# Performance work log

Measured on AMD Instinct MI355X. Metric: run time of the kernel, lower is better.

Reference implementation:

```python
import jax, jax.numpy as jnp
import numpy as np

B, S, D = 2, 512, 256      # batch, seq_len, d_model
N = 16                     # d_state
DC = 4                     # d_conv
DI = 2 * D                 # d_inner
CHUNK = 32                 # scan remat chunk size (S % CHUNK == 0)


def setup_inputs() -> dict:
    key = jax.random.key(0)
    ks = jax.random.split(key, 10)
    sc = 0.02
    return {
        "x": jax.random.normal(ks[0], (B, S, D), jnp.float32),
        "adjacency_matrix": jax.random.uniform(ks[1], (B, S, S), dtype=jnp.float32),
        "ln_w": jnp.ones((D,), jnp.float32),
        "ln_b": jnp.zeros((D,), jnp.float32),
        "W_in": jax.random.normal(ks[2], (2 * DI, D), jnp.float32) * sc,
        "conv_w": jax.random.normal(ks[3], (DI, DI, DC), jnp.float32) * sc,
        "conv_b": jnp.zeros((DI,), jnp.float32),
        "W_xp": jax.random.normal(ks[4], (2 * N + 1, DI), jnp.float32) * sc,
        "W_dt": jax.random.normal(ks[5], (DI, 1), jnp.float32) * sc,
        "b_dt": jnp.zeros((DI,), jnp.float32),
        "Wr": jax.random.normal(ks[6], (N, N), jnp.float32) * sc,
        "br": jnp.zeros((N,), jnp.float32),
        "W_out": jax.random.normal(ks[7], (D, DI), jnp.float32) * sc,
    }


def _forward(x, adj, ln_w, ln_b, W_in, conv_w, conv_b, W_xp, W_dt, b_dt, Wr, br, W_out):
    residual = x
    # LayerNorm (biased variance, eps=1e-5, matching nn.LayerNorm)
    mu = x.mean(-1, keepdims=True)
    var = ((x - mu) ** 2).mean(-1, keepdims=True)
    xn = (x - mu) * jax.lax.rsqrt(var + 1e-5) * ln_w + ln_b
    # in_proj (no bias), chunk into x branch and gate z
    xz = xn @ W_in.T                                  # [B,S,2*DI]
    xp, z = xz[..., :DI], xz[..., DI:]
    # causal-ish conv1d with padding d_conv-1, then slice to seq_len
    xc = jax.lax.conv_general_dilated(
        xp.transpose(0, 2, 1), conv_w, (1,), [(DC - 1, DC - 1)],
        dimension_numbers=("NCH", "OIH", "NCH"))
    xc = (xc + conv_b[None, :, None])[..., :S].transpose(0, 2, 1)  # [B,S,DI]
    x_act = jax.nn.silu(xc)
    # x_proj (no bias) -> delta(1), B(N), C(N)
    ssm = x_act @ W_xp.T                              # [B,S,2N+1]
    delta = jax.nn.softplus(ssm[..., :1] @ W_dt.T + b_dt)  # [B,S,DI]
    Bm, Cm = ssm[..., 1:1 + N], ssm[..., 1 + N:]      # [B,S,N]
    pos = jnp.arange(S)

    def step(carry, xs):
        h, hist = xs_carry = carry
        t, d_t, B_t, C_t, x_t, a_t = xs
        # exponential-decay state update: h [B,DI,N]
        h = h * jnp.exp(-d_t)[..., None] + x_t[..., None] * B_t[:, None, :]
        # adjacency-gated, degree-normalized aggregation over prior states
        w = a_t * (pos < t)                           # [B,S], zeros for s>=t
        deg = jnp.maximum(w.sum(-1), 1.0)             # clamp(min=1.0)
        g = jnp.einsum('bs,sbdn->bdn', w, hist) / deg[:, None, None]
        boost = 0.1 * jax.nn.silu(g @ Wr.T + br)
        # torch skips the boost when t==0 or all causal weights are zero
        h = h + jnp.where((t > 0) & jnp.any(w > 0), boost, jnp.zeros_like(boost))
        hist = hist.at[t].set(h)
        y = jnp.einsum('bdn,bn->bd', h, C_t)
        return (h, hist), y

    xs = (pos,
          delta.transpose(1, 0, 2), Bm.transpose(1, 0, 2), Cm.transpose(1, 0, 2),
          x_act.transpose(1, 0, 2), adj.transpose(1, 0, 2))
    nchunks = S // CHUNK
    xs = jax.tree_util.tree_map(lambda a: a.reshape(nchunks, CHUNK, *a.shape[1:]), xs)
    carry0 = (jnp.zeros((B, DI, N), jnp.float32),
              jnp.zeros((S, B, DI, N), jnp.float32))

    @jax.checkpoint
    def chunk_body(carry, xs_c):
        return jax.lax.scan(step, carry, xs_c)

    _, ys = jax.lax.scan(chunk_body, carry0, xs)
    y = ys.reshape(S, B, DI).transpose(1, 0, 2)       # [B,S,DI]
    return (y * jax.nn.silu(z)) @ W_out.T + residual


def reference(x, adjacency_matrix, ln_w, ln_b, W_in, conv_w, conv_b, W_xp, W_dt, b_dt, Wr, br, W_out):
    return _forward(x, adjacency_matrix, ln_w, ln_b, W_in, conv_w, conv_b,
                    W_xp, W_dt, b_dt, Wr, br, W_out)
```

## Files before the change

kernel.cpp:

```cpp
#include <hip/hip_runtime.h>
#include <math.h>

static constexpr int B  = 2;
static constexpr int S  = 512;
static constexpr int D  = 256;
static constexpr int N  = 16;
static constexpr int DI = 512;
static constexpr int CHUNK = 32;
static constexpr int NCHUNK = S / CHUNK;
static constexpr int NL = NCHUNK / 2;
static constexpr int DN = DI * N;

typedef unsigned int uint32;
typedef unsigned short ushort16;
using bf16x8 = __attribute__((ext_vector_type(8))) short;
using f32x4  = __attribute__((ext_vector_type(4))) float;

__device__ __forceinline__ ushort16 f2bf(float f) {
    uint32 u = __float_as_uint(f);
    u = (u + 0x7fffu + ((u >> 16) & 1u)) >> 16;
    return (ushort16)u;
}
__device__ __forceinline__ float bflo(uint32 u) { return __uint_as_float(u << 16); }
__device__ __forceinline__ float bfhi(uint32 u) { return __uint_as_float(u & 0xffff0000u); }
__device__ __forceinline__ float bf2f(ushort16 u) { return __uint_as_float(((uint32)u) << 16); }
__device__ __forceinline__ uint32 pk2(float a, float b) {
    return (uint32)(ushort16)f2bf(a) | ((uint32)(ushort16)f2bf(b) << 16);
}
template<int K>
__device__ __forceinline__ float rork(float x) {
    return __uint_as_float((uint32)__builtin_amdgcn_mov_dpp(
        (int)__float_as_uint(x), 0x120 + K, 0xf, 0xf, false));
}

__global__ void ln_k(const float* __restrict__ x, const float* __restrict__ w,
                     const float* __restrict__ bias, ushort16* __restrict__ xnb) {
    int row = blockIdx.x;
    int lane = threadIdx.x;
    float4 v = *(const float4*)(x + row * D + lane * 4);
    float s = v.x + v.y + v.z + v.w;
    float q = v.x * v.x + v.y * v.y + v.z * v.z + v.w * v.w;
    for (int m = 1; m < 64; m <<= 1) { s += __shfl_xor(s, m); q += __shfl_xor(q, m); }
    float mu  = s * (1.0f / D);
    float var = q * (1.0f / D) - mu * mu;
    float rs  = rsqrtf(var + 1e-5f);
    float4 wv = *(const float4*)(w + lane * 4);
    float4 bv = *(const float4*)(bias + lane * 4);
    float4 o;
    o.x = (v.x - mu) * rs * wv.x + bv.x;
    o.y = (v.y - mu) * rs * wv.y + bv.y;
    o.z = (v.z - mu) * rs * wv.z + bv.z;
    o.w = (v.w - mu) * rs * wv.w + bv.w;
    uint2 pk;
    pk.x = pk2(o.x, o.y);
    pk.y = pk2(o.z, o.w);
    *(uint2*)(xnb + row * D + lane * 4) = pk;
}

template<int MODE>
__global__ __launch_bounds__(256) void gemmb_k(const ushort16* __restrict__ A,
                                               const float* __restrict__ W,
                                               const float* __restrict__ res,
                                               float* __restrict__ C,
                                               ushort16* __restrict__ xpb,
                                               float* __restrict__ zs,
                                               int M, int Nc, int K) {
    __shared__ __align__(16) short As[64 * 40];
    __shared__ __align__(16) short Ws[64 * 40];
    int tid = threadIdx.x;
    int l = tid & 63, wid = tid >> 6;
    int wm = wid & 1, wn = wid >> 1;
    int row0 = blockIdx.y * 64, col0 = blockIdx.x * 64;
    int r = tid >> 2, kseg = (tid & 3) * 8;
    f32x4 acc[2][2] = {};
    for (int k0 = 0; k0 < K; k0 += 32) {
        *(uint4*)&As[r * 40 + kseg] = *(const uint4*)(A + (size_t)(row0 + r) * K + k0 + kseg);
        {
            const float* wrow = W + (size_t)(col0 + r) * K + k0 + kseg;
            float4 w0 = *(const float4*)wrow;
            float4 w1 = *(const float4*)(wrow + 4);
            uint4 q;
            q.x = pk2(w0.x, w0.y); q.y = pk2(w0.z, w0.w);
            q.z = pk2(w1.x, w1.y); q.w = pk2(w1.z, w1.w);
            *(uint4*)&Ws[r * 40 + kseg] = q;
        }
        __syncthreads();
        bf16x8 aF[2], bF[2];
        #pragma unroll
        for (int am = 0; am < 2; ++am)
            aF[am] = *(const bf16x8*)&As[(wm * 32 + am * 16 + (l & 15)) * 40 + (l >> 4) * 8];
        #pragma unroll
        for (int bn = 0; bn < 2; ++bn)
            bF[bn] = *(const bf16x8*)&Ws[(wn * 32 + bn * 16 + (l & 15)) * 40 + (l >> 4) * 8];
        #pragma unroll
        for (int am = 0; am < 2; ++am)
            #pragma unroll
            for (int bn = 0; bn < 2; ++bn)
                acc[am][bn] = __builtin_amdgcn_mfma_f32_16x16x32_bf16(aF[am], bF[bn], acc[am][bn], 0, 0, 0);
        __syncthreads();
    }
    #pragma unroll
    for (int am = 0; am < 2; ++am)
        #pragma unroll
        for (int bn = 0; bn < 2; ++bn) {
            int cc = col0 + wn * 32 + bn * 16 + (l & 15);
            #pragma unroll
            for (int reg = 0; reg < 4; ++reg) {
                int rr = row0 + wm * 32 + am * 16 + (l >> 4) * 4 + reg;
                float v = acc[am][bn][reg];
                if (MODE == 0) {
                    if (res) v += res[(size_t)rr * Nc + cc];
                    C[(size_t)rr * Nc + cc] = v;
                } else {
                    int b = rr >> 9, t = rr & (S - 1);
                    if (cc < DI)
                        xpb[((size_t)(b * (S + 3) + 3 + t)) * DI + cc] = f2bf(v);
                    else
                        zs[((size_t)(b * S + t)) * DI + (cc - DI)] = v / (1.0f + __expf(-v));
                }
            }
        }
}

__global__ __launch_bounds__(256) void convm_k(const ushort16* __restrict__ xpb,
                                               const float* __restrict__ conv_w,
                                               const float* __restrict__ conv_b,
                                               float* __restrict__ x_act) {
    __shared__ __align__(16) short AxS[35 * 40];
    __shared__ __align__(16) short WbS[4 * 32 * 40];
    int tid = threadIdx.x;
    int l = tid & 63, wid = tid >> 6;
    int wm = wid & 1, wn = wid >> 1;
    int o0 = blockIdx.x * 32;
    int mt = blockIdx.y;
    int b = mt >> 4, tl0 = (mt & 15) * 32;
    f32x4 acc = {0.f, 0.f, 0.f, 0.f};

    for (int k0 = 0; k0 < DI; k0 += 32) {
        if (tid < 140) {
            int rr = tid >> 2, seg = tid & 3;
            uint4 v = *(const uint4*)(xpb + ((size_t)(b * (S + 3) + tl0 + rr)) * DI + k0 + seg * 8);
            *(uint4*)&AxS[rr * 40 + seg * 8] = v;
        }
        #pragma unroll
        for (int it = 0; it < 4; ++it) {
            int p = it * 256 + tid;
            int o = p >> 5, i = p & 31;
            float4 w4 = *(const float4*)(conv_w + ((size_t)(o0 + o) * DI + (k0 + i)) * 4);
            WbS[(0 * 32 + o) * 40 + i] = (short)f2bf(w4.x);
            WbS[(1 * 32 + o) * 40 + i] = (short)f2bf(w4.y);
            WbS[(2 * 32 + o) * 40 + i] = (short)f2bf(w4.z);
            WbS[(3 * 32 + o) * 40 + i] = (short)f2bf(w4.w);
        }
        __syncthreads();
        #pragma unroll
        for (int k = 0; k < 4; ++k) {
            bf16x8 aF = *(const bf16x8*)&AxS[(wm * 16 + (l & 15) + k) * 40 + (l >> 4) * 8];
            bf16x8 bF = *(const bf16x8*)&WbS[(k * 32 + wn * 16 + (l & 15)) * 40 + (l >> 4) * 8];
            acc = __builtin_amdgcn_mfma_f32_16x16x32_bf16(aF, bF, acc, 0, 0, 0);
        }
        __syncthreads();
    }
    int oc = o0 + wn * 16 + (l & 15);
    float bia = conv_b[oc];
    #pragma unroll
    for (int reg = 0; reg < 4; ++reg) {
        int m = wm * 16 + (l >> 4) * 4 + reg;
        float v = acc[reg] + bia;
        x_act[((size_t)(b * S + tl0 + m)) * DI + oc] = v / (1.0f + __expf(-v));
    }
}

__global__ void ssmE_k(const float* __restrict__ x_act, const float* __restrict__ W_xp,
                       const float* __restrict__ W_dt, const float* __restrict__ b_dt,
                       float* __restrict__ Bm, float* __restrict__ Cm,
                       float* __restrict__ E) {
    int row = blockIdx.x * 4 + (threadIdx.x >> 6);
    int lane = threadIdx.x & 63;
    const float* xr = x_act + (size_t)row * DI + lane * 8;
    float4 v0 = *(const float4*)xr;
    float4 v1 = *(const float4*)(xr + 4);
    float dtr = 0.0f;
    for (int j = 0; j < 2 * N + 1; ++j) {
        const float* wr = W_xp + (size_t)j * DI + lane * 8;
        float4 w0 = *(const float4*)wr;
        float4 w1 = *(const float4*)(wr + 4);
        float acc = v0.x * w0.x + v0.y * w0.y + v0.z * w0.z + v0.w * w0.w
                  + v1.x * w1.x + v1.y * w1.y + v1.z * w1.z + v1.w * w1.w;
        for (int m = 1; m < 64; m <<= 1) acc += __shfl_xor(acc, m);
        if (j == 0) dtr = acc;
        if (lane == 0) {
            if (j >= 1 && j < 1 + N) Bm[(size_t)row * N + (j - 1)] = acc;
            else if (j >= 1 + N)     Cm[(size_t)row * N + (j - 1 - N)] = acc;
        }
    }
    int d0 = lane * 8;
    float4 w0 = *(const float4*)(W_dt + d0);
    float4 w1 = *(const float4*)(W_dt + d0 + 4);
    float4 q0 = *(const float4*)(b_dt + d0);
    float4 q1 = *(const float4*)(b_dt + d0 + 4);
    float4 e0, e1;
    e0.x = 1.0f / (1.0f + __expf(dtr * w0.x + q0.x));
    e0.y = 1.0f / (1.0f + __expf(dtr * w0.y + q0.y));
    e0.z = 1.0f / (1.0f + __expf(dtr * w0.z + q0.z));
    e0.w = 1.0f / (1.0f + __expf(dtr * w0.w + q0.w));
    e1.x = 1.0f / (1.0f + __expf(dtr * w1.x + q1.x));
    e1.y = 1.0f / (1.0f + __expf(dtr * w1.y + q1.y));
    e1.z = 1.0f / (1.0f + __expf(dtr * w1.z + q1.z));
    e1.w = 1.0f / (1.0f + __expf(dtr * w1.w + q1.w));
    *(float4*)(E + (size_t)row * DI + d0) = e0;
    *(float4*)(E + (size_t)row * DI + d0 + 4) = e1;
}

__global__ void deg_k(const float* __restrict__ adj, float* __restrict__ rdeg, int* __restrict__ flagI) {
    int t = blockIdx.x & (S - 1), b = blockIdx.x >> 9;
    int lane = threadIdx.x;
    const float* row = adj + ((size_t)(b * S + t)) * S;
    float s = 0.0f; bool anyp = false;
    for (int i = lane; i < t; i += 64) { float v = row[i]; s += v; anyp |= (v > 0.0f); }
    for (int m = 1; m < 64; m <<= 1) s += __shfl_xor(s, m);
    bool any = __any(anyp);
    if (lane == 0) {
        rdeg[b * S + t] = 1.0f / fmaxf(s, 1.0f);
        if (t > 0 && any) atomicOr(flagI + t, 1);
    }
}

#define SCAN32(RO, ADJT, GSUM)                                              \
    _Pragma("unroll")                                                       \
    for (int j = 0; j < CHUNK; ++j) {                                       \
        float e  = eL [((RO) + j) * 8 + grp];                               \
        float xa = xaL[((RO) + j) * 8 + grp];                               \
        float Bn = BnL[((RO) + j) * 16 + n];                                \
        h = h * e + xa * Bn;                                                \
        float g0 = GSUM[j], g1 = 0.f, g2 = 0.f, g3 = 0.f;                   \
        const float* ar = (ADJT) + j * 36;                                  \
        int sp = 0;                                                         \
        _Pragma("unroll")                                                   \
        for (; sp + 4 <= j; sp += 4) {                                      \
            float4 av = *(const float4*)(ar + sp);                          \
            g0 += av.x * hreg[sp];     g1 += av.y * hreg[sp + 1];           \
            g2 += av.z * hreg[sp + 2]; g3 += av.w * hreg[sp + 3];           \
        }                                                                   \
        _Pragma("unroll")                                                   \
        for (; sp < j; ++sp) g0 += ar[sp] * hreg[sp];                       \
        float gr = (g0 + g1) + (g2 + g3);                                   \
        float m0 = gr * wrr[0] + rork<4>(gr) * wrr[4]                       \
                 + rork<8>(gr) * wrr[8] + rork<12>(gr) * wrr[12];           \
        float m1 = rork<1>(gr) * wrr[1] + rork<5>(gr) * wrr[5]              \
                 + rork<9>(gr) * wrr[9] + rork<13>(gr) * wrr[13];           \
        float m2 = rork<2>(gr) * wrr[2] + rork<6>(gr) * wrr[6]              \
                 + rork<10>(gr) * wrr[10] + rork<14>(gr) * wrr[14];         \
        float m3 = rork<3>(gr) * wrr[3] + rork<7>(gr) * wrr[7]              \
                 + rork<11>(gr) * wrr[11] + rork<15>(gr) * wrr[15];         \
        float acc = fmaf(rdegL[(RO) + j], (m0 + m1) + (m2 + m3), brn);      \
        if (flL[(RO) + j]) h += 0.1f * acc / (1.0f + __expf(-acc));         \
        hreg[j] = h;                                                        \
    }

#define PRESUM(GSUM, PTR) {                                                 \
    const ushort16* _p = (PTR);                                             \
    _Pragma("unroll")                                                       \
    for (int qi = 0; qi < 4; ++qi) {                                        \
        uint4 q = *(const uint4*)(_p + qi * 8);                             \
        GSUM[qi*8+0] += bflo(q.x); GSUM[qi*8+1] += bfhi(q.x);               \
        GSUM[qi*8+2] += bflo(q.y); GSUM[qi*8+3] += bfhi(q.y);               \
        GSUM[qi*8+4] += bflo(q.z); GSUM[qi*8+5] += bfhi(q.z);               \
        GSUM[qi*8+6] += bflo(q.w); GSUM[qi*8+7] += bfhi(q.w);               \
    } }

__global__ __launch_bounds__(256) void chunk2_k(const float* __restrict__ adj,
                                                const float* __restrict__ x_act,
                                                const float* __restrict__ E,
                                                const float* __restrict__ Bm,
                                                const float* __restrict__ rdeg,
                                                const int* __restrict__ flagI,
                                                const float* __restrict__ Wr,
                                                const float* __restrict__ br,
                                                ushort16* __restrict__ Gall,
                                                ushort16* __restrict__ histT,
                                                float* __restrict__ hlast, int lc) {
    __shared__ __align__(16) char smem[56320];
    int tid = threadIdx.x;
    int cbA = 2 * lc * CHUNK;
    int cbB = cbA + CHUNK;
    const size_t SLOT = (size_t)B * DN * 32;
    int rp = lc & 1, wp = (lc + 1) & 1;

    if (blockIdx.x < 128) {
        float* adjA  = (float*)smem;
        float* adjB  = (float*)(smem + 4608);
        short* AsM   = (short*)(smem + 9216);
        short* AsT   = (short*)(smem + 11776);
        float* eL    = (float*)(smem + 22016);
        float* xaL   = (float*)(smem + 24064);
        float* BnL   = (float*)(smem + 26112);
        float* rdegL = (float*)(smem + 30208);
        int*   flL   = (int*)  (smem + 30464);
        short* hTA   = (short*)(smem + 31232);
        float* Gmid  = (float*)(smem + 39424);
        short* hTB   = (short*)(smem + 39424);

        int b = blockIdx.x >> 6;
        int d0 = (blockIdx.x & 63) << 3;
        int n = tid & 15, grp = tid >> 4;
        int d = d0 + (grp & 7);
        int dn = d * N + n;
        int dnbase = (blockIdx.x & 63) << 7;

        {
            int j = tid >> 3, s4 = (tid & 7) * 4;
            {
                float4 a0 = *(const float4*)(adj + ((size_t)(b * S + cbA + j)) * S + cbA + s4);
                float* dp = adjA + j * 36 + s4;
                dp[0] = a0.x; dp[1] = a0.y; dp[2] = a0.z; dp[3] = a0.w;
            }
            {
                float4 a0 = *(const float4*)(adj + ((size_t)(b * S + cbB + j)) * S + cbB + s4);
                float* dp = adjB + j * 36 + s4;
                dp[0] = a0.x; dp[1] = a0.y; dp[2] = a0.z; dp[3] = a0.w;
            }
            {
                float4 a0 = *(const float4*)(adj + ((size_t)(b * S + cbB + j)) * S + cbA + s4);
                uint2 q; q.x = pk2(a0.x, a0.y); q.y = pk2(a0.z, a0.w);
                *(uint2*)&AsM[j * 40 + s4] = q;
            }
            if (lc < NL - 1) {
                #pragma unroll
                for (int st = 0; st < 4; ++st) {
                    int src = st >> 1, tgt = st & 1;
                    float4 a0 = *(const float4*)(adj + ((size_t)(b * S + cbA + 64 + 32 * tgt + j)) * S
                                                 + cbA + 32 * src + s4);
                    uint2 q; q.x = pk2(a0.x, a0.y); q.y = pk2(a0.z, a0.w);
                    *(uint2*)&AsT[(src * 2 + tgt) * 1280 + j * 40 + s4] = q;
                }
            }
            int jr = tid >> 2, dd = (tid & 3) * 2;
            float2 ev = *(const float2*)(E     + ((size_t)(b * S + cbA + jr)) * DI + d0 + dd);
            float2 xv = *(const float2*)(x_act + ((size_t)(b * S + cbA + jr)) * DI + d0 + dd);
            eL [jr * 8 + dd] = ev.x; eL [jr * 8 + dd + 1] = ev.y;
            xaL[jr * 8 + dd] = xv.x; xaL[jr * 8 + dd + 1] = xv.y;
            int nn = (tid & 3) * 4;
            float4 bv = *(const float4*)(Bm + ((size_t)(b * S + cbA + jr)) * N + nn);
            BnL[jr * 16 + nn] = bv.x; BnL[jr * 16 + nn + 1] = bv.y;
            BnL[jr * 16 + nn + 2] = bv.z; BnL[jr * 16 + nn + 3] = bv.w;
            if (tid < 64) {
                rdegL[tid] = rdeg[b * S + cbA + tid];
                flL[tid]   = flagI[cbA + tid];
            }
        }
        __syncthreads();
        if (tid >= 128) return;

        float gsA[CHUNK], gsB[CHUNK];
        #pragma unroll
        for (int j = 0; j < CHUNK; ++j) { gsA[j] = 0.f; gsB[j] = 0.f; }
        {
            size_t tb = ((size_t)b * DN + dn) * 32;
            if (lc >= 2) {
                PRESUM(gsA, Gall + ((size_t)rp * 6 + 0) * SLOT + tb);
                PRESUM(gsB, Gall + ((size_t)rp * 6 + 1) * SLOT + tb);
            }
            if (lc >= 1) {
                PRESUM(gsA, Gall + ((size_t)rp * 6 + 2) * SLOT + tb);
                PRESUM(gsA, Gall + ((size_t)rp * 6 + 4) * SLOT + tb);
                PRESUM(gsB, Gall + ((size_t)rp * 6 + 3) * SLOT + tb);
                PRESUM(gsB, Gall + ((size_t)rp * 6 + 5) * SLOT + tb);
            }
        }

        int probe = __builtin_amdgcn_mov_dpp((int)n, 0x121, 0xf, 0xf, false);
        bool plusdir = (probe == ((n + 1) & 15));
        float wrr[16];
        #pragma unroll
        for (int k = 0; k < 16; ++k) {
            int ip = (n + k) & 15, im = (n - k + 16) & 15;
            wrr[k] = Wr[n * 16 + (plusdir ? ip : im)];
        }
        float brn = br[n];
        float h = (lc == 0) ? 0.0f : hlast[b * DN + dn];

        float hreg[CHUNK];
        SCAN32(0, adjA, gsA)

        {
            ushort16* ht = histT + ((size_t)b * DN + dn) * S + cbA;
            #pragma unroll
            for (int qi = 0; qi < 4; ++qi) {
                uint4 q;
                q.x = pk2(hreg[qi*8+0], hreg[qi*8+1]);
                q.y = pk2(hreg[qi*8+2], hreg[qi*8+3]);
                q.z = pk2(hreg[qi*8+4], hreg[qi*8+5]);
                q.w = pk2(hreg[qi*8+6], hreg[qi*8+7]);
                *(uint4*)(ht + qi * 8) = q;
                *(uint4*)&hTA[qi * 1024 + tid * 8] = q;
            }
        }
        __syncthreads();
        {
            int w = tid >> 6, l = tid & 63;
            bf16x8 aF0 = *(const bf16x8*)&AsM[(l & 15) * 40 + (l >> 4) * 8];
            bf16x8 aF1 = *(const bf16x8*)&AsM[(16 + (l & 15)) * 40 + (l >> 4) * 8];
            #pragma unroll
            for (int dblk = 0; dblk < 4; ++dblk) {
                int col = w * 64 + dblk * 16 + (l & 15);
                bf16x8 bF = *(const bf16x8*)&hTA[(l >> 4) * 1024 + col * 8];
                f32x4 a0v = {0.f,0.f,0.f,0.f}, a1v = {0.f,0.f,0.f,0.f};
                a0v = __builtin_amdgcn_mfma_f32_16x16x32_bf16(aF0, bF, a0v, 0, 0, 0);
                a1v = __builtin_amdgcn_mfma_f32_16x16x32_bf16(aF1, bF, a1v, 0, 0, 0);
                int jb0 = (l >> 4) * 4;
                #pragma unroll
                for (int reg = 0; reg < 4; ++reg) {
                    Gmid[(jb0 + reg) * 129 + col]      = a0v[reg];
                    Gmid[(16 + jb0 + reg) * 129 + col] = a1v[reg];
                }
            }
        }
        __syncthreads();
        #pragma unroll
        for (int j = 0; j < CHUNK; ++j) gsB[j] += Gmid[j * 129 + tid];
        __syncthreads();

        SCAN32(32, adjB, gsB)
        hlast[b * DN + dn] = h;

        {
            ushort16* ht = histT + ((size_t)b * DN + dn) * S + cbB;
            #pragma unroll
            for (int qi = 0; qi < 4; ++qi) {
                uint4 q;
                q.x = pk2(hreg[qi*8+0], hreg[qi*8+1]);
                q.y = pk2(hreg[qi*8+2], hreg[qi*8+3]);
                q.z = pk2(hreg[qi*8+4], hreg[qi*8+5]);
                q.w = pk2(hreg[qi*8+6], hreg[qi*8+7]);
                *(uint4*)(ht + qi * 8) = q;
                *(uint4*)&hTB[qi * 1024 + tid * 8] = q;
            }
        }
        if (lc < NL - 1) {
            __syncthreads();
            int w = tid >> 6, l = tid & 63;
            int jb0 = (l >> 4) * 4;
            #pragma unroll
            for (int src = 0; src < 2; ++src) {
                const short* hTs = src ? hTB : hTA;
                #pragma unroll
                for (int tgt = 0; tgt < 2; ++tgt) {
                    const short* At = AsT + (src * 2 + tgt) * 1280;
                    bf16x8 aF0 = *(const bf16x8*)&At[(l & 15) * 40 + (l >> 4) * 8];
                    bf16x8 aF1 = *(const bf16x8*)&At[(16 + (l & 15)) * 40 + (l >> 4) * 8];
                    ushort16* gw = Gall + ((size_t)wp * 6 + (2 + src * 2 + tgt)) * SLOT;
                    #pragma unroll
                    for (int dblk = 0; dblk < 4; ++dblk) {
                        int col = w * 64 + dblk * 16 + (l & 15);
                        bf16x8 bF = *(const bf16x8*)&hTs[(l >> 4) * 1024 + col * 8];
                        f32x4 a0v = {0.f,0.f,0.f,0.f}, a1v = {0.f,0.f,0.f,0.f};
                        a0v = __builtin_amdgcn_mfma_f32_16x16x32_bf16(aF0, bF, a0v, 0, 0, 0);
                        a1v = __builtin_amdgcn_mfma_f32_16x16x32_bf16(aF1, bF, a1v, 0, 0, 0);
                        int dng = dnbase + col;
                        uint2 o0, o1;
                        o0.x = pk2(a0v[0], a0v[1]); o0.y = pk2(a0v[2], a0v[3]);
                        o1.x = pk2(a1v[0], a1v[1]); o1.y = pk2(a1v[2], a1v[3]);
                        *(uint2*)(gw + ((size_t)b * DN + dng) * 32 + jb0) = o0;
                        *(uint2*)(gw + ((size_t)b * DN + dng) * 32 + 16 + jb0) = o1;
                    }
                }
            }
        }
    } else {
        if (lc == 0 || lc >= NL - 1) return;
        int idx = blockIdx.x - 128;
        int tile = idx & 63;
        int b = (idx >> 6) & 1;
        int tgt = idx >> 7;
        int tc = 2 * lc + 2 + tgt;
        int dn0 = tile * 128;
        int w = tid >> 6, l = tid & 63;
        int jh = w & 1, dh = w >> 1;
        int kseg = (l >> 4) * 8;
        const float* abase = adj + ((size_t)(b * S + tc * CHUNK + jh * 16 + (l & 15))) * S + kseg;
        const ushort16* hbase = histT + ((size_t)b * DN + dn0 + dh * 64 + (l & 15)) * S + kseg;
        int K = 2 * lc;
        f32x4 acc[4] = {};
        #pragma unroll 2
        for (int ks = 0; ks < K; ++ks) {
            float4 af0 = *(const float4*)(abase + ks * 32);
            float4 af1 = *(const float4*)(abase + ks * 32 + 4);
            uint4 aP;
            aP.x = pk2(af0.x, af0.y); aP.y = pk2(af0.z, af0.w);
            aP.z = pk2(af1.x, af1.y); aP.w = pk2(af1.z, af1.w);
            bf16x8 aF;
            *(uint4*)&aF = aP;
            uint4 bP[4];
            #pragma unroll
            for (int dblk = 0; dblk < 4; ++dblk)
                bP[dblk] = *(const uint4*)(hbase + (size_t)(dblk * 16) * S + ks * 32);
            #pragma unroll
            for (int dblk = 0; dblk < 4; ++dblk) {
                bf16x8 bF;
                *(uint4*)&bF = bP[dblk];
                acc[dblk] = __builtin_amdgcn_mfma_f32_16x16x32_bf16(aF, bF, acc[dblk], 0, 0, 0);
            }
        }
        int jb = jh * 16 + (l >> 4) * 4;
        ushort16* gbase = Gall + ((size_t)wp * 6 + tgt) * SLOT;
        #pragma unroll
        for (int dblk = 0; dblk < 4; ++dblk) {
            int dnc = dn0 + dh * 64 + dblk * 16 + (l & 15);
            uint2 o;
            o.x = pk2(acc[dblk][0], acc[dblk][1]);
            o.y = pk2(acc[dblk][2], acc[dblk][3]);
            *(uint2*)(gbase + ((size_t)b * DN + dnc) * 32 + jb) = o;
        }
    }
}

__global__ __launch_bounds__(256) void y_k(const ushort16* __restrict__ histT,
                                           const float* __restrict__ Cm,
                                           const float* __restrict__ zs,
                                           ushort16* __restrict__ yzb) {
    __shared__ float CmL[S * 17];
    int b = blockIdx.x >> 9;
    int d = blockIdx.x & (DI - 1);
    int tid = threadIdx.x;
    #pragma unroll
    for (int q = 0; q < 8; ++q) {
        int l0 = q * 1024 + tid * 4;
        int t = l0 >> 4, n0 = l0 & 15;
        float4 v = *(const float4*)(Cm + (size_t)b * S * N + l0);
        CmL[t * 17 + n0]     = v.x;
        CmL[t * 17 + n0 + 1] = v.y;
        CmL[t * 17 + n0 + 2] = v.z;
        CmL[t * 17 + n0 + 3] = v.w;
    }
    __syncthreads();
    const ushort16* hbase = histT + ((size_t)b * DN + d * N) * S;
    #pragma unroll
    for (int pass = 0; pass < 2; ++pass) {
        int t = pass * 256 + tid;
        float a0 = 0.f, a1 = 0.f, a2 = 0.f, a3 = 0.f;
        #pragma unroll
        for (int n = 0; n < 16; n += 4) {
            a0 += bf2f(hbase[(size_t)n * S + t])       * CmL[t * 17 + n];
            a1 += bf2f(hbase[(size_t)(n + 1) * S + t]) * CmL[t * 17 + n + 1];
            a2 += bf2f(hbase[(size_t)(n + 2) * S + t]) * CmL[t * 17 + n + 2];
            a3 += bf2f(hbase[(size_t)(n + 3) * S + t]) * CmL[t * 17 + n + 3];
        }
        float acc = (a0 + a1) + (a2 + a3);
        float zv = zs[((size_t)(b * S + t)) * DI + d];
        yzb[((size_t)(b * S + t)) * DI + d] = f2bf(acc * zv);
    }
}

extern "C" void kernel_launch(void* const* d_in, const int* in_sizes, int n_in,
                              void* d_out, int out_size, void* d_ws, size_t ws_size,
                              hipStream_t stream) {
    const float* x      = (const float*)d_in[0];
    const float* adj    = (const float*)d_in[1];
    const float* ln_w   = (const float*)d_in[2];
    const float* ln_b   = (const float*)d_in[3];
    const float* W_in   = (const float*)d_in[4];
    const float* conv_w = (const float*)d_in[5];
    const float* conv_b = (const float*)d_in[6];
    const float* W_xp   = (const float*)d_in[7];
    const float* W_dt   = (const float*)d_in[8];
    const float* b_dt   = (const float*)d_in[9];
    const float* Wr     = (const float*)d_in[10];
    const float* br     = (const float*)d_in[11];
    const float* W_out  = (const float*)d_in[12];
    float* out = (float*)d_out;

    float* ws = (float*)d_ws;
    size_t off = 0;
    float* x_act  = ws + off; off += (size_t)B * S * DI;
    float* Bmb    = ws + off; off += (size_t)B * S * N;
    float* Cmb    = ws + off; off += (size_t)B * S * N;
    float* rdegp  = ws + off; off += (size_t)B * S;
    int*   flagI  = (int*)(ws + off); off += S;
    float* Ebuf   = ws + off; off += (size_t)B * S * DI;
    float* zsbuf  = ws + off; off += (size_t)B * S * DI;
    float* hlast  = ws + off; off += (size_t)B * DN;
    ushort16* xnb    = (ushort16*)(ws + off); off += (size_t)B * S * D / 2;
    ushort16* yzb    = (ushort16*)(ws + off); off += (size_t)B * S * DI / 2;
    ushort16* histT  = (ushort16*)(ws + off); off += (size_t)B * DN * S / 2;
    ushort16* Gall   = (ushort16*)(ws + off); off += (size_t)2 * 6 * B * DN * 32 / 2;
    ushort16* xpb    = (ushort16*)(ws + off); off += (size_t)B * (S + 3) * DI / 2;

    hipMemsetAsync(flagI, 0, S * sizeof(int), stream);
    hipMemsetAsync(xpb, 0, (size_t)B * (S + 3) * DI * 2, stream);

    ln_k<<<B * S, 64, 0, stream>>>(x, ln_w, ln_b, xnb);
    gemmb_k<1><<<dim3(2 * DI / 64, B * S / 64), 256, 0, stream>>>(
        xnb, W_in, nullptr, nullptr, xpb, zsbuf, B * S, 2 * DI, D);
    convm_k<<<dim3(DI / 32, B * S / 32), 256, 0, stream>>>(xpb, conv_w, conv_b, x_act);
    ssmE_k<<<B * S / 4, 256, 0, stream>>>(x_act, W_xp, W_dt, b_dt, Bmb, Cmb, Ebuf);
    deg_k<<<B * S, 64, 0, stream>>>(adj, rdegp, flagI);

    for (int lc = 0; lc < NL; ++lc)
        chunk2_k<<<384, 256, 0, stream>>>(adj, x_act, Ebuf, Bmb, rdegp, flagI,
                                          Wr, br, Gall, histT, hlast, lc);

    y_k<<<B * DI, 256, 0, stream>>>(histT, Cmb, zsbuf, yzb);

    gemmb_k<0><<<dim3(D / 64, B * S / 64), 256, 0, stream>>>(
        yzb, W_out, x, out, nullptr, nullptr, B * S, D, DI);
}
```

Baseline: 277.8 us.

## Split history GEMM K-range across two block sets and retile histT by chunk

The long-range history GEMM blocks in chunk2_k now split their K loop into two halves, handled by separate blocks that write separate Gall slots. The per-step scan reads both slots. The grid grows from 384 to 640 blocks so more CUs share the work that grows with lc. histT is relaid out as [b][chunk][dn][32] so each chunk's history is contiguous for the MFMA loads and stores. The scan's silu boost also switches to an fma with a hardware reciprocal. The costs are extra partial-sum reads and a larger Gall buffer.

```diff
diff --git a/kernel.cpp b/kernel.cpp
--- a/kernel.cpp
+++ b/kernel.cpp
@@ -10,6 +10,7 @@
 static constexpr int NCHUNK = S / CHUNK;
 static constexpr int NL = NCHUNK / 2;
 static constexpr int DN = DI * N;
+static constexpr int NSLOT = 8;
 
 typedef unsigned int uint32;
 typedef unsigned short ushort16;
@@ -31,6 +32,9 @@
 __device__ __forceinline__ float rork(float x) {
     return __uint_as_float((uint32)__builtin_amdgcn_mov_dpp(
         (int)__float_as_uint(x), 0x120 + K, 0xf, 0xf, false));
+}
+__device__ __forceinline__ size_t htIdx(int b, int dn, int sb) {
+    return ((size_t)(b * (S / 32) + sb) * DN + dn) * 32;
 }
 
 __global__ void ln_k(const float* __restrict__ x, const float* __restrict__ w,
@@ -254,7 +258,9 @@
         float m3 = rork<3>(gr) * wrr[3] + rork<7>(gr) * wrr[7]              \
                  + rork<11>(gr) * wrr[11] + rork<15>(gr) * wrr[15];         \
         float acc = fmaf(rdegL[(RO) + j], (m0 + m1) + (m2 + m3), brn);      \
-        if (flL[(RO) + j]) h += 0.1f * acc / (1.0f + __expf(-acc));         \
+        if (flL[(RO) + j])                                                  \
+            h = fmaf(0.1f * acc,                                            \
+                     __builtin_amdgcn_rcpf(1.0f + __expf(-acc)), h);        \
         hreg[j] = h;                                                        \
     }
 
@@ -358,14 +364,16 @@
         {
             size_t tb = ((size_t)b * DN + dn) * 32;
             if (lc >= 2) {
-                PRESUM(gsA, Gall + ((size_t)rp * 6 + 0) * SLOT + tb);
-                PRESUM(gsB, Gall + ((size_t)rp * 6 + 1) * SLOT + tb);
+                PRESUM(gsA, Gall + ((size_t)rp * NSLOT + 0) * SLOT + tb);
+                PRESUM(gsA, Gall + ((size_t)rp * NSLOT + 1) * SLOT + tb);
+                PRESUM(gsB, Gall + ((size_t)rp * NSLOT + 2) * SLOT + tb);
+                PRESUM(gsB, Gall + ((size_t)rp * NSLOT + 3) * SLOT + tb);
             }
             if (lc >= 1) {
-                PRESUM(gsA, Gall + ((size_t)rp * 6 + 2) * SLOT + tb);
-                PRESUM(gsA, Gall + ((size_t)rp * 6 + 4) * SLOT + tb);
-                PRESUM(gsB, Gall + ((size_t)rp * 6 + 3) * SLOT + tb);
-                PRESUM(gsB, Gall + ((size_t)rp * 6 + 5) * SLOT + tb);
+                PRESUM(gsA, Gall + ((size_t)rp * NSLOT + 4) * SLOT + tb);
+                PRESUM(gsA, Gall + ((size_t)rp * NSLOT + 6) * SLOT + tb);
+                PRESUM(gsB, Gall + ((size_t)rp * NSLOT + 5) * SLOT + tb);
+                PRESUM(gsB, Gall + ((size_t)rp * NSLOT + 7) * SLOT + tb);
             }
         }
 
@@ -384,7 +392,7 @@
         SCAN32(0, adjA, gsA)
 
         {
-            ushort16* ht = histT + ((size_t)b * DN + dn) * S + cbA;
+            ushort16* ht = histT + htIdx(b, dn, 2 * lc);
             #pragma unroll
             for (int qi = 0; qi < 4; ++qi) {
                 uint4 q;
@@ -425,7 +433,7 @@
         hlast[b * DN + dn] = h;
 
         {
-            ushort16* ht = histT + ((size_t)b * DN + dn) * S + cbB;
+            ushort16* ht = histT + htIdx(b, dn, 2 * lc + 1);
             #pragma unroll
             for (int qi = 0; qi < 4; ++qi) {
                 uint4 q;
@@ -449,7 +457,7 @@
                     const short* At = AsT + (src * 2 + tgt) * 1280;
                     bf16x8 aF0 = *(const bf16x8*)&At[(l & 15) * 40 + (l >> 4) * 8];
                     bf16x8 aF1 = *(const bf16x8*)&At[(16 + (l & 15)) * 40 + (l >> 4) * 8];
-                    ushort16* gw = Gall + ((size_t)wp * 6 + (2 + src * 2 + tgt)) * SLOT;
+                    ushort16* gw = Gall + ((size_t)wp * NSLOT + (4 + src * 2 + tgt)) * SLOT;
                     #pragma unroll
                     for (int dblk = 0; dblk < 4; ++dblk) {
                         int col = w * 64 + dblk * 16 + (l & 15);
@@ -472,18 +480,20 @@
         int idx = blockIdx.x - 128;
         int tile = idx & 63;
         int b = (idx >> 6) & 1;
-        int tgt = idx >> 7;
+        int tgt = (idx >> 7) & 1;
+        int kh = idx >> 8;
         int tc = 2 * lc + 2 + tgt;
+        int ks0 = kh ? lc : 0;
+        int ks1 = kh ? 2 * lc : lc;
         int dn0 = tile * 128;
         int w = tid >> 6, l = tid & 63;
         int jh = w & 1, dh = w >> 1;
         int kseg = (l >> 4) * 8;
         const float* abase = adj + ((size_t)(b * S + tc * CHUNK + jh * 16 + (l & 15))) * S + kseg;
-        const ushort16* hbase = histT + ((size_t)b * DN + dn0 + dh * 64 + (l & 15)) * S + kseg;
-        int K = 2 * lc;
+        int dnrow = dn0 + dh * 64 + (l & 15);
         f32x4 acc[4] = {};
         #pragma unroll 2
-        for (int ks = 0; ks < K; ++ks) {
+        for (int ks = ks0; ks < ks1; ++ks) {
             float4 af0 = *(const float4*)(abase + ks * 32);
             float4 af1 = *(const float4*)(abase + ks * 32 + 4);
             uint4 aP;
@@ -494,7 +504,7 @@
             uint4 bP[4];
             #pragma unroll
             for (int dblk = 0; dblk < 4; ++dblk)
-                bP[dblk] = *(const uint4*)(hbase + (size_t)(dblk * 16) * S + ks * 32);
+                bP[dblk] = *(const uint4*)(histT + htIdx(b, dnrow + dblk * 16, ks) + kseg);
             #pragma unroll
             for (int dblk = 0; dblk < 4; ++dblk) {
                 bf16x8 bF;
@@ -503,7 +513,7 @@
             }
         }
         int jb = jh * 16 + (l >> 4) * 4;
-        ushort16* gbase = Gall + ((size_t)wp * 6 + tgt) * SLOT;
+        ushort16* gbase = Gall + ((size_t)wp * NSLOT + (tgt * 2 + kh)) * SLOT;
         #pragma unroll
         for (int dblk = 0; dblk < 4; ++dblk) {
             int dnc = dn0 + dh * 64 + dblk * 16 + (l & 15);
@@ -534,17 +544,18 @@
         CmL[t * 17 + n0 + 3] = v.w;
     }
     __syncthreads();
-    const ushort16* hbase = histT + ((size_t)b * DN + d * N) * S;
     #pragma unroll
     for (int pass = 0; pass < 2; ++pass) {
         int t = pass * 256 + tid;
+        int sb = t >> 5, si = t & 31;
+        const ushort16* hb = histT + htIdx(b, d * N, sb) + si;
         float a0 = 0.f, a1 = 0.f, a2 = 0.f, a3 = 0.f;
         #pragma unroll
         for (int n = 0; n < 16; n += 4) {
-            a0 += bf2f(hbase[(size_t)n * S + t])       * CmL[t * 17 + n];
-            a1 += bf2f(hbase[(size_t)(n + 1) * S + t]) * CmL[t * 17 + n + 1];
-            a2 += bf2f(hbase[(size_t)(n + 2) * S + t]) * CmL[t * 17 + n + 2];
-            a3 += bf2f(hbase[(size_t)(n + 3) * S + t]) * CmL[t * 17 + n + 3];
+            a0 += bf2f(hb[(size_t)n * 32])       * CmL[t * 17 + n];
+            a1 += bf2f(hb[(size_t)(n + 1) * 32]) * CmL[t * 17 + n + 1];
+            a2 += bf2f(hb[(size_t)(n + 2) * 32]) * CmL[t * 17 + n + 2];
+            a3 += bf2f(hb[(size_t)(n + 3) * 32]) * CmL[t * 17 + n + 3];
         }
         float acc = (a0 + a1) + (a2 + a3);
         float zv = zs[((size_t)(b * S + t)) * DI + d];
@@ -583,7 +594,7 @@
     ushort16* xnb    = (ushort16*)(ws + off); off += (size_t)B * S * D / 2;
     ushort16* yzb    = (ushort16*)(ws + off); off += (size_t)B * S * DI / 2;
     ushort16* histT  = (ushort16*)(ws + off); off += (size_t)B * DN * S / 2;
-    ushort16* Gall   = (ushort16*)(ws + off); off += (size_t)2 * 6 * B * DN * 32 / 2;
+    ushort16* Gall   = (ushort16*)(ws + off); off += (size_t)2 * NSLOT * B * DN * 32 / 2;
     ushort16* xpb    = (ushort16*)(ws + off); off += (size_t)B * (S + 3) * DI / 2;
 
     hipMemsetAsync(flagI, 0, S * sizeof(int), stream);
@@ -597,7 +608,7 @@
     deg_k<<<B * S, 64, 0, stream>>>(adj, rdegp, flagI);
 
     for (int lc = 0; lc < NL; ++lc)
-        chunk2_k<<<384, 256, 0, stream>>>(adj, x_act, Ebuf, Bmb, rdegp, flagI,
+        chunk2_k<<<640, 256, 0, stream>>>(adj, x_act, Ebuf, Bmb, rdegp, flagI,
                                           Wr, br, Gall, histT, hlast, lc);
 
     y_k<<<B * DI, 256, 0, stream>>>(histT, Cmb, zsbuf, yzb);
```

After: 265.5 us. 4.4% less time.
